# Kernel optimization log

Measured on AMD Instinct MI355X. Metric: run time of the kernel, lower is better.

## Reference

```python
import jax, jax.numpy as jnp
import numpy as np

N_STEPS = 128
DT = 0.001
TAU_M = 10.0 * DT            # NeuroTorch LIFLayer default tau_m = 10*dt
ALPHA = float(np.exp(-DT / TAU_M))
THRESHOLD = 1.0
GAMMA = 100.0                # surrogate-gradient sharpness

@jax.custom_vjp
def spike_fn(v):
    # Heaviside spike with sigmoid surrogate gradient (HeavisideSigmoidApprox)
    return (v >= THRESHOLD).astype(v.dtype)

def _spike_fwd(v):
    return spike_fn(v), v

def _spike_bwd(v, g):
    s = jax.nn.sigmoid(GAMMA * (v - THRESHOLD))
    return (g * GAMMA * s * (1.0 - s),)

spike_fn.defvjp(_spike_fwd, _spike_bwd)

def setup_inputs() -> dict:
    key = jax.random.key(0)
    B, N = 256, 2048
    x = jax.random.normal(key, (B, N), dtype=jnp.float32)
    W = jnp.eye(N, dtype=jnp.float32)  # default forward_weights = eye(n_units)
    return {"x": x, "W": W}

def reference(x, W):
    B, N = x.shape
    # ConstantValuesTransform repeats x over all n_steps, so the input current
    # I = x @ W is identical every step; hoist it out of the scan.
    I = x @ W  # [B, N]
    V0 = jnp.zeros((B, N), dtype=x.dtype)
    Z0 = jnp.zeros((B, N), dtype=x.dtype)

    def step(carry, _):
        V, Z = carry
        # reset via previous spikes (detached in original: Z.detach())
        V_next = (ALPHA * V + I) * (1.0 - jax.lax.stop_gradient(Z))
        Z_next = spike_fn(V_next)
        return (V_next, Z_next), Z_next

    _, spikes = jax.lax.scan(step, (V0, Z0), None, length=N_STEPS)  # [T, B, N]
    return jnp.transpose(spikes, (1, 0, 2))  # [B, T, N] like torch.stack(dim=1)
```

## Files before the change

kernel.cpp:

```cpp
#include <hip/hip_runtime.h>
#include <cstddef>

#define Mdim 256
#define Ndim 2048
#define Kdim 2048
#define Tsteps 128

typedef float v4f __attribute__((ext_vector_type(4)));

__global__ __launch_bounds__(256) void scan_w_kernel(
    const float* __restrict__ W, unsigned char* __restrict__ flags)
{
    const int c = blockIdx.x;
    const int g = blockIdx.y;
    const int tid = threadIdx.x;

    __shared__ int wmask[4];

    const int coff = (tid & 31) * 4;
    const int rbase = tid >> 5;

    unsigned mask = 0;
#pragma unroll
    for (int it = 0; it < 16; ++it) {
        const int r = it * 8 + rbase;
        const float4 v = *(const float4*)&W[(size_t)(g * 128 + r) * Ndim + c * 128 + coff];
        const bool nz = (v.x != 0.0f) | (v.y != 0.0f) | (v.z != 0.0f) | (v.w != 0.0f);
        mask |= (nz ? 1u : 0u) << (it >> 1);
    }
#pragma unroll
    for (int off = 32; off; off >>= 1) mask |= __shfl_down(mask, off);
    if ((tid & 63) == 0) wmask[tid >> 6] = (int)mask;
    __syncthreads();
    if (tid == 0) {
        const int m = wmask[0] | wmask[1] | wmask[2] | wmask[3];
        flags[c * 16 + g] = (unsigned char)m;
    }
}

__global__ __launch_bounds__(256, 2) void lif_fused_kernel(
    const float* __restrict__ x, const float* __restrict__ W,
    const unsigned* __restrict__ flags, float* __restrict__ out)
{
    __shared__ float xs[Kdim];

    const int tid = threadIdx.x;
    const int b = blockIdx.x >> 1;
    const int n = ((blockIdx.x & 1) << 10) + tid * 4;
    const int c = n >> 7;

    {
        const float* xp = x + (size_t)b * Kdim;
        *(float4*)&xs[tid * 4]        = *(const float4*)&xp[tid * 4];
        *(float4*)&xs[1024 + tid * 4] = *(const float4*)&xp[1024 + tid * 4];
    }
    __syncthreads();

    float f0 = 0.0f, f1 = 0.0f, f2 = 0.0f, f3 = 0.0f;
#pragma unroll
    for (int w = 0; w < 4; ++w) {
        unsigned word = flags[c * 4 + w];
        while (word) {
            const int bit = __builtin_ctz(word);
            word &= word - 1;
            const int k0 = (w * 32 + bit) * 16;
            const float* wp = W + (size_t)k0 * Ndim + n;
#pragma unroll
            for (int kk = 0; kk < 16; ++kk) {
                const float xv = xs[k0 + kk];
                const float4 wv = *(const float4*)(wp + (size_t)kk * Ndim);
                f0 = fmaf(xv, wv.x, f0);
                f1 = fmaf(xv, wv.y, f1);
                f2 = fmaf(xv, wv.z, f2);
                f3 = fmaf(xv, wv.w, f3);
            }
        }
    }
    const float Iv[4] = {f0, f1, f2, f3};

    const float ALPHA = (float)0.9048374180359595;

    unsigned zb[4][4] = {{0u, 0u, 0u, 0u}, {0u, 0u, 0u, 0u},
                         {0u, 0u, 0u, 0u}, {0u, 0u, 0u, 0u}};
    float V[4] = {0.0f, 0.0f, 0.0f, 0.0f};
    float Z[4] = {0.0f, 0.0f, 0.0f, 0.0f};
#pragma unroll
    for (int w = 0; w < 4; ++w) {
#pragma unroll
        for (int t2 = 0; t2 < 32; ++t2) {
#pragma unroll
            for (int j = 0; j < 4; ++j) {
                float v = __fmul_rn(ALPHA, V[j]);
                v = __fadd_rn(v, Iv[j]);
                v = __fmul_rn(v, __fsub_rn(1.0f, Z[j]));
                V[j] = v;
                const bool sp = (v >= 1.0f);
                Z[j] = sp ? 1.0f : 0.0f;
                zb[j][w] |= sp ? (1u << t2) : 0u;
            }
        }
    }

    float* op = out + (size_t)b * Tsteps * Ndim + n;
#pragma unroll
    for (int w = 0; w < 4; ++w) {
#pragma unroll
        for (int t2 = 0; t2 < 32; ++t2) {
            v4f s = { (float)((zb[0][w] >> t2) & 1u),
                      (float)((zb[1][w] >> t2) & 1u),
                      (float)((zb[2][w] >> t2) & 1u),
                      (float)((zb[3][w] >> t2) & 1u) };
            __builtin_nontemporal_store(s, (v4f*)(op + (size_t)(w * 32 + t2) * Ndim));
        }
    }
}

extern "C" void kernel_launch(void* const* d_in, const int* in_sizes, int n_in,
                              void* d_out, int out_size, void* d_ws, size_t ws_size,
                              hipStream_t stream) {
    const float* x = (const float*)d_in[0];
    const float* W = (const float*)d_in[1];
    float* out = (float*)d_out;

    unsigned char* flags = (unsigned char*)d_ws;

    scan_w_kernel<<<dim3(16, 16), 256, 0, stream>>>(W, flags);

    const int sim_blocks = Mdim * Ndim / 1024;
    lif_fused_kernel<<<dim3(sim_blocks), 256, 0, stream>>>(
        x, W, (const unsigned*)flags, out);
}
```

Measured before the change: 289.1 us.

## Split fused kernel into register-tiled current GEMM and separate LIF scan

Moves the sparse-block x@W computation into its own kernel, where each thread computes four rows by two columns so each W load is reused across four batch rows. The result goes through a workspace buffer that a separate LIF simulation kernel reads. The reset step also now uses a boolean select instead of multiplying by (1-Z). The aim is to cut redundant W traffic, at the cost of an extra launch and an I round trip through global memory.

```diff
diff --git a/kernel.cpp b/kernel.cpp
--- a/kernel.cpp
+++ b/kernel.cpp
@@ -38,25 +38,29 @@
     }
 }
 
-__global__ __launch_bounds__(256, 2) void lif_fused_kernel(
+__global__ __launch_bounds__(256, 2) void current_kernel(
     const float* __restrict__ x, const float* __restrict__ W,
-    const unsigned* __restrict__ flags, float* __restrict__ out)
+    const unsigned* __restrict__ flags, float* __restrict__ I)
 {
-    __shared__ float xs[Kdim];
-
     const int tid = threadIdx.x;
-    const int b = blockIdx.x >> 1;
-    const int n = ((blockIdx.x & 1) << 10) + tid * 4;
+    const int r0 = blockIdx.x * 4;
+    const int n0 = blockIdx.y * 512;
+    const int n = n0 + tid * 2;
     const int c = n >> 7;
 
+    __shared__ float xs[4][Kdim];
+
     {
-        const float* xp = x + (size_t)b * Kdim;
-        *(float4*)&xs[tid * 4]        = *(const float4*)&xp[tid * 4];
-        *(float4*)&xs[1024 + tid * 4] = *(const float4*)&xp[1024 + tid * 4];
+        const float* xp = x + (size_t)r0 * Kdim;
+#pragma unroll
+        for (int r = 0; r < 4; ++r) {
+            *(float4*)&xs[r][tid * 4]        = *(const float4*)&xp[(size_t)r * Kdim + tid * 4];
+            *(float4*)&xs[r][1024 + tid * 4] = *(const float4*)&xp[(size_t)r * Kdim + 1024 + tid * 4];
+        }
     }
     __syncthreads();
 
-    float f0 = 0.0f, f1 = 0.0f, f2 = 0.0f, f3 = 0.0f;
+    float acc[4][2] = {{0.0f, 0.0f}, {0.0f, 0.0f}, {0.0f, 0.0f}, {0.0f, 0.0f}};
 #pragma unroll
     for (int w = 0; w < 4; ++w) {
         unsigned word = flags[c * 4 + w];
@@ -67,36 +71,49 @@
             const float* wp = W + (size_t)k0 * Ndim + n;
 #pragma unroll
             for (int kk = 0; kk < 16; ++kk) {
-                const float xv = xs[k0 + kk];
-                const float4 wv = *(const float4*)(wp + (size_t)kk * Ndim);
-                f0 = fmaf(xv, wv.x, f0);
-                f1 = fmaf(xv, wv.y, f1);
-                f2 = fmaf(xv, wv.z, f2);
-                f3 = fmaf(xv, wv.w, f3);
+                const float2 wv = *(const float2*)(wp + (size_t)kk * Ndim);
+#pragma unroll
+                for (int r = 0; r < 4; ++r) {
+                    const float xv = xs[r][k0 + kk];
+                    acc[r][0] = fmaf(xv, wv.x, acc[r][0]);
+                    acc[r][1] = fmaf(xv, wv.y, acc[r][1]);
+                }
             }
         }
     }
-    const float Iv[4] = {f0, f1, f2, f3};
+#pragma unroll
+    for (int r = 0; r < 4; ++r)
+        *(float2*)&I[(size_t)(r0 + r) * Ndim + n] = *(const float2*)acc[r];
+}
+
+__global__ __launch_bounds__(256, 2) void lif_kernel(
+    const float* __restrict__ I, float* __restrict__ out)
+{
+    const int tid = threadIdx.x;
+    const int b = blockIdx.x >> 1;
+    const int n = ((blockIdx.x & 1) << 10) + tid * 4;
+
+    const float4 iv4 = *(const float4*)&I[(size_t)b * Ndim + n];
+    const float Iv[4] = {iv4.x, iv4.y, iv4.z, iv4.w};
 
     const float ALPHA = (float)0.9048374180359595;
 
     unsigned zb[4][4] = {{0u, 0u, 0u, 0u}, {0u, 0u, 0u, 0u},
                          {0u, 0u, 0u, 0u}, {0u, 0u, 0u, 0u}};
     float V[4] = {0.0f, 0.0f, 0.0f, 0.0f};
-    float Z[4] = {0.0f, 0.0f, 0.0f, 0.0f};
+    bool Zp[4] = {false, false, false, false};
 #pragma unroll
     for (int w = 0; w < 4; ++w) {
 #pragma unroll
         for (int t2 = 0; t2 < 32; ++t2) {
 #pragma unroll
             for (int j = 0; j < 4; ++j) {
-                float v = __fmul_rn(ALPHA, V[j]);
-                v = __fadd_rn(v, Iv[j]);
-                v = __fmul_rn(v, __fsub_rn(1.0f, Z[j]));
+                const float u = __fadd_rn(__fmul_rn(ALPHA, V[j]), Iv[j]);
+                const float v = Zp[j] ? 0.0f : u;
                 V[j] = v;
                 const bool sp = (v >= 1.0f);
-                Z[j] = sp ? 1.0f : 0.0f;
                 zb[j][w] |= sp ? (1u << t2) : 0u;
+                Zp[j] = sp;
             }
         }
     }
@@ -123,10 +140,13 @@
     float* out = (float*)d_out;
 
     unsigned char* flags = (unsigned char*)d_ws;
+    float* Ibuf = (float*)((char*)d_ws + 4096);
 
     scan_w_kernel<<<dim3(16, 16), 256, 0, stream>>>(W, flags);
 
+    current_kernel<<<dim3(Mdim / 4, Ndim / 512), 256, 0, stream>>>(
+        x, W, (const unsigned*)flags, Ibuf);
+
     const int sim_blocks = Mdim * Ndim / 1024;
-    lif_fused_kernel<<<dim3(sim_blocks), 256, 0, stream>>>(
-        x, W, (const unsigned*)flags, out);
+    lif_kernel<<<dim3(sim_blocks), 256, 0, stream>>>(Ibuf, out);
 }
```

Measured after the change: 291.9 us. No clear change (+1.0%).
